# Performance work log

Hardware: AMD Instinct MI355X
Metric: run time of the kernel (lower is better)

Reference implementation:

```python
import jax, jax.numpy as jnp
import numpy as np

B, S, D = 1, 2048, 1024
H, HD = 16, 64            # attn_num, head dim (D = H*HD)
TE, K, ED = 16, 2, 512    # experts, top_k, expert_dim
DS = 2048                 # shared_expert_dim
EPS = 1e-5
THETA = 10000.0
RSF = 1.0                 # routed_scaling_factor


def rmsnorm(x, w):
    return x * jax.lax.rsqrt(jnp.mean(x * x, axis=-1, keepdims=True) + EPS) * w


def rope(x):
    # x: [B,H,S,a]; half-split rotary as in RotaryEmb
    a = x.shape[-1]
    inv = (1.0 / THETA) ** (jnp.arange(0, a, 2, dtype=jnp.float32) / a)
    fr = jnp.outer(jnp.arange(x.shape[2], dtype=jnp.float32), inv)[None, None]  # [1,1,S,a/2]
    c, s = jnp.cos(fr), jnp.sin(fr)
    x1, x2 = jnp.split(x, 2, axis=-1)
    return jnp.concatenate([x1 * c + x2 * s, -x1 * s + x2 * c], axis=-1)


def setup_inputs() -> dict:
    key = jax.random.key(0)
    ks = jax.random.split(key, 16)
    w = 0.02
    return {
        "x_input": jax.random.normal(ks[0], (B, S, D), jnp.float32),
        "indices": jax.random.randint(ks[1], (B * S, K), 0, TE),
        "values": jax.random.normal(ks[2], (B * S, K), jnp.float32),
        "attn_w": jax.random.normal(ks[3], (3 * D, D), jnp.float32) * w,
        "attn_o_w": jax.random.normal(ks[4], (D, D), jnp.float32) * w,
        "attn_norm_w": jnp.ones((D,), jnp.float32),
        "ffn_norm_w": jnp.ones((D,), jnp.float32),
        "ffn_experts": jax.random.normal(ks[5], (3, TE, D, ED), jnp.float32) * w,
        "main_keys": jax.random.normal(ks[6], (D, TE), jnp.float32) * w,
        "main_bias": jnp.zeros((TE,), jnp.float32),
        "output_coeff": jnp.ones((1, 1, D), jnp.float32),
        "ffn_up_w": jax.random.normal(ks[7], (2 * DS, D), jnp.float32) * w,
        "ffn_down_w": jax.random.normal(ks[8], (D, DS), jnp.float32) * w,
        "shared_norm_w": jnp.ones((D,), jnp.float32),
    }


def reference(x_input, indices, values, attn_w, attn_o_w, attn_norm_w, ffn_norm_w,
              ffn_experts, main_keys, main_bias, output_coeff, ffn_up_w,
              ffn_down_w, shared_norm_w):
    # --- attention block ---
    x = rmsnorm(x_input, attn_norm_w)
    qkv = x @ attn_w.T                                  # [B,S,3D]
    xq, xk, xv = jnp.split(qkv, 3, axis=-1)
    def heads(t):
        return t.reshape(B, S, H, HD).transpose(0, 2, 1, 3)  # [B,H,S,HD]
    q, k, v = rope(heads(xq)), rope(heads(xk)), heads(xv)
    att = jnp.einsum('bhqa,bhka->bhqk', q, k) / jnp.sqrt(jnp.float32(HD))
    causal = jnp.tril(jnp.ones((S, S), bool))
    att = jnp.where(causal, att, jnp.finfo(att.dtype).min)
    att = jax.nn.softmax(att, axis=-1)
    o = jnp.einsum('bhqk,bhka->bhqa', att, v)
    x_attn = o.transpose(0, 2, 1, 3).reshape(B, S, D)
    x_ffn_input = x_attn @ attn_o_w.T + x_input

    # --- router ---
    x_ffn = rmsnorm(x_ffn_input, ffn_norm_w)
    T = B * S
    token_values = (x_ffn @ main_keys).reshape(T, TE)
    tv = jnp.take_along_axis(token_values, indices, axis=-1)  # [T,K]
    vals = values + tv + main_bias[indices]
    scores = jax.nn.softmax(vals, axis=-1) * RSF              # [T,K]

    # --- grouped GEMM experts (SwiGLU), dense combine over experts ---
    combine = jnp.zeros((T, TE), x_ffn.dtype).at[
        jnp.arange(T)[:, None], indices].add(scores)          # [T,TE]
    xf = x_ffn.reshape(T, D)
    h1 = jnp.einsum('td,edh->eth', xf, ffn_experts[0])
    h2 = jnp.einsum('td,edh->eth', xf, ffn_experts[1])
    g = jax.nn.silu(h1) * h2                                  # [TE,T,ED]
    ye = jnp.einsum('eth,edh->etd', g, ffn_experts[2])        # [TE,T,D]
    y = jnp.einsum('etd,te->td', ye, combine).reshape(B, S, D)
    y = y * output_coeff

    # --- shared SwiGLU expert ---
    x1, x2 = jnp.split(x_ffn @ ffn_up_w.T, 2, axis=-1)
    y_shared = (jax.nn.silu(x1) * x2) @ ffn_down_w.T
    y_shared = rmsnorm(y_shared, shared_norm_w)

    return y + y_shared + x_ffn_input
```

## Files before the change

kernel.cpp:

```cpp
#include <hip/hip_runtime.h>
#include <hip/hip_bf16.h>

using bf16 = __hip_bfloat16;

#define S_   2048
#define D_   1024
#define H_   16
#define HD_  64
#define TE_  16
#define ED_  512
#define DS_  2048
#define CAP_ 512

#define NEG_ -1e30f

typedef __attribute__((ext_vector_type(8))) short bf16x8;
typedef __attribute__((ext_vector_type(4))) float f32x4;
#define MFMA16(a, b, c) __builtin_amdgcn_mfma_f32_16x16x32_bf16(a, b, c, 0, 0, 0)

__device__ __forceinline__ void storeF(float* p, float v) { *p = v; }
__device__ __forceinline__ void storeF(bf16* p, float v)  { *p = __float2bfloat16(v); }
__device__ __forceinline__ short cvt1(float f) {
    bf16 h = __float2bfloat16(f);
    return *(short*)&h;
}
__device__ __forceinline__ float b2f(short s) {
    return __uint_as_float(((unsigned)(unsigned short)s) << 16);
}

__device__ __forceinline__ void load16(const bf16* g, short* l) {
    __builtin_amdgcn_global_load_lds(
        (const __attribute__((address_space(1))) unsigned*)g,
        (__attribute__((address_space(3))) unsigned*)l, 16, 0, 0);
}

__global__ __launch_bounds__(256) void convert_kernel(
        const float* __restrict__ src, bf16* __restrict__ dst)
{
    const size_t i = ((size_t)blockIdx.x*256 + threadIdx.x)*8;
    const float4 f0 = *(const float4*)(src + i);
    const float4 f1 = *(const float4*)(src + i + 4);
    short t8[8];
    t8[0]=cvt1(f0.x); t8[1]=cvt1(f0.y); t8[2]=cvt1(f0.z); t8[3]=cvt1(f0.w);
    t8[4]=cvt1(f1.x); t8[5]=cvt1(f1.y); t8[6]=cvt1(f1.z); t8[7]=cvt1(f1.w);
    *(bf16x8*)(dst + i) = *(bf16x8*)t8;
}

__global__ __launch_bounds__(256) void mkT_kernel(
        const float* __restrict__ mk, float* __restrict__ mkT)
{
    const int idx = blockIdx.x*256 + threadIdx.x;
    const int e = idx >> 10, d = idx & 1023;
    mkT[idx] = mk[d*TE_ + e];
}

__global__ __launch_bounds__(256) void rmsnorm_kernel(
        const float* __restrict__ x, const float* __restrict__ w,
        bf16* __restrict__ out)
{
    const int t = blockIdx.x, tid = threadIdx.x;
    __shared__ float red[4];
    float xv[4];
    float ss = 0.f;
#pragma unroll
    for (int i = 0; i < 4; ++i) {
        xv[i] = x[(size_t)t*D_ + tid + 256*i];
        ss += xv[i]*xv[i];
    }
#pragma unroll
    for (int off = 32; off; off >>= 1) ss += __shfl_xor(ss, off, 64);
    if ((tid & 63) == 0) red[tid >> 6] = ss;
    __syncthreads();
    const float rn = rsqrtf((red[0]+red[1]+red[2]+red[3]) * (1.f/D_) + 1e-5f);
#pragma unroll
    for (int i = 0; i < 4; ++i) {
        const int d = tid + 256*i;
        out[(size_t)t*D_ + d] = __float2bfloat16(xv[i] * rn * w[d]);
    }
}

template<typename OutT, bool HAS_RES>
__global__ __launch_bounds__(256) void gemm_mfma_bb_kernel(
    const bf16* __restrict__ A, const bf16* __restrict__ B,
    OutT* __restrict__ C, const float* __restrict__ Res,
    int M, int N, int K)
{
    __shared__ short As[128*32];
    __shared__ short Bs[128*32];
    const int tid = threadIdx.x;
    const int w = tid >> 6, l = tid & 63;
    const int wm = w >> 1, wn = w & 1;
    const int m0 = blockIdx.y * 128, n0 = blockIdx.x * 128;
    const int lr = l >> 2, lq = l & 3;
    const int fm = l & 15, fq = l >> 4;
    f32x4 acc[4][4];
#pragma unroll
    for (int i = 0; i < 4; ++i)
#pragma unroll
        for (int j = 0; j < 4; ++j) acc[i][j] = (f32x4){0.f,0.f,0.f,0.f};

    const bf16* ga = A + (size_t)(m0 + w*16 + lr)*K + lq*8;
    const bf16* gb = B + (size_t)(n0 + w*16 + lr)*K + lq*8;
    for (int k0 = 0; k0 < K; k0 += 32) {
        load16(ga + k0,                &As[(w*16)*32]);
        load16(ga + k0 + (size_t)64*K, &As[(64 + w*16)*32]);
        load16(gb + k0,                &Bs[(w*16)*32]);
        load16(gb + k0 + (size_t)64*K, &Bs[(64 + w*16)*32]);
        __syncthreads();
        bf16x8 af[4], bfr[4];
#pragma unroll
        for (int mi = 0; mi < 4; ++mi)
            af[mi] = *(const bf16x8*)&As[(wm*64 + mi*16 + fm)*32 + fq*8];
#pragma unroll
        for (int ni = 0; ni < 4; ++ni)
            bfr[ni] = *(const bf16x8*)&Bs[(wn*64 + ni*16 + fm)*32 + fq*8];
#pragma unroll
        for (int mi = 0; mi < 4; ++mi)
#pragma unroll
            for (int ni = 0; ni < 4; ++ni)
                acc[mi][ni] = MFMA16(af[mi], bfr[ni], acc[mi][ni]);
        __syncthreads();
    }
#pragma unroll
    for (int mi = 0; mi < 4; ++mi)
#pragma unroll
        for (int ni = 0; ni < 4; ++ni)
#pragma unroll
            for (int r = 0; r < 4; ++r) {
                const int row = m0 + wm*64 + mi*16 + fq*4 + r;
                const int col = n0 + wn*64 + ni*16 + fm;
                float v = acc[mi][ni][r];
                if constexpr (HAS_RES) v += Res[(size_t)row*N + col];
                storeF(&C[(size_t)row*N + col], v);
            }
}

__global__ __launch_bounds__(256) void transpose_kernel(
    const float* __restrict__ src, bf16* __restrict__ dst)
{
    __shared__ bf16 tile[64][65];
    const int h0 = blockIdx.x*64, d0 = blockIdx.y*64, m = blockIdx.z;
    const float* s = src + (size_t)m*D_*ED_;
    bf16*        o = dst + (size_t)m*ED_*D_;
    const int tid = threadIdx.x;
#pragma unroll
    for (int i = 0; i < 16; ++i) {
        const int idx = tid + 256*i;
        const int r = idx >> 6, c = idx & 63;
        tile[r][c] = __float2bfloat16(s[(size_t)(d0 + r)*ED_ + h0 + c]);
    }
    __syncthreads();
#pragma unroll
    for (int i = 0; i < 16; ++i) {
        const int idx = tid + 256*i;
        const int r = idx >> 6, c = idx & 63;
        o[(size_t)(h0 + r)*D_ + d0 + c] = tile[c][r];
    }
}

__global__ __launch_bounds__(256) void expert_mid_mfma_kernel(
    const bf16* __restrict__ xffn, const bf16* __restrict__ w0t,
    const int* __restrict__ counts, const int* __restrict__ pairs,
    const float* __restrict__ pw, bf16* __restrict__ gbuf)
{
    const int ht = blockIdx.x, pt = blockIdx.y, e = blockIdx.z;
    const int cnt = counts[e];
    if (pt*128 >= cnt) return;
    __shared__ short Xs[128*32];
    __shared__ short W0s[64*32];
    __shared__ short W1s[64*32];
    __shared__ int   toks[128];
    __shared__ float wrow[128];
    const int tid = threadIdx.x;
    const int w = tid >> 6, l = tid & 63;
    const int wm = w >> 1, wn = w & 1;
    const int lr = l >> 2, lq = l & 3;
    const int fm = l & 15, fq = l >> 4;
    if (tid < 128) {
        const int p = pt*128 + tid;
        if (p < cnt) { toks[tid] = pairs[e*CAP_ + p] >> 1; wrow[tid] = pw[e*CAP_ + p]; }
        else         { toks[tid] = 0;                      wrow[tid] = 0.f; }
    }
    __syncthreads();
    const int t0 = toks[w*16 + lr], t1 = toks[64 + w*16 + lr];
    const bf16* gx0 = xffn + (size_t)t0*D_ + lq*8;
    const bf16* gx1 = xffn + (size_t)t1*D_ + lq*8;
    const bf16* g0  = w0t + ((size_t)e*ED_ + ht*64 + w*16 + lr)*D_ + lq*8;
    const bf16* g1  = w0t + ((size_t)(16 + e)*ED_ + ht*64 + w*16 + lr)*D_ + lq*8;
    f32x4 acc1[4][2], acc2[4][2];
#pragma unroll
    for (int i = 0; i < 4; ++i)
#pragma unroll
        for (int j = 0; j < 2; ++j) {
            acc1[i][j] = (f32x4){0.f,0.f,0.f,0.f};
            acc2[i][j] = (f32x4){0.f,0.f,0.f,0.f};
        }
    for (int k0 = 0; k0 < D_; k0 += 32) {
        load16(gx0 + k0, &Xs[(w*16)*32]);
        load16(gx1 + k0, &Xs[(64 + w*16)*32]);
        load16(g0 + k0,  &W0s[(w*16)*32]);
        load16(g1 + k0,  &W1s[(w*16)*32]);
        __syncthreads();
        bf16x8 af[4], b0[2], b1[2];
#pragma unroll
        for (int mi = 0; mi < 4; ++mi)
            af[mi] = *(const bf16x8*)&Xs[(wm*64 + mi*16 + fm)*32 + fq*8];
#pragma unroll
        for (int ni = 0; ni < 2; ++ni) {
            b0[ni] = *(const bf16x8*)&W0s[(wn*32 + ni*16 + fm)*32 + fq*8];
            b1[ni] = *(const bf16x8*)&W1s[(wn*32 + ni*16 + fm)*32 + fq*8];
        }
#pragma unroll
        for (int mi = 0; mi < 4; ++mi)
#pragma unroll
            for (int ni = 0; ni < 2; ++ni) {
                acc1[mi][ni] = MFMA16(af[mi], b0[ni], acc1[mi][ni]);
                acc2[mi][ni] = MFMA16(af[mi], b1[ni], acc2[mi][ni]);
            }
        __syncthreads();
    }
#pragma unroll
    for (int mi = 0; mi < 4; ++mi)
#pragma unroll
        for (int ni = 0; ni < 2; ++ni)
#pragma unroll
            for (int r = 0; r < 4; ++r) {
                const int row = wm*64 + mi*16 + fq*4 + r;
                const int col = wn*32 + ni*16 + fm;
                const float h1 = acc1[mi][ni][r], h2 = acc2[mi][ni][r];
                const float g = wrow[row] * (h1 / (1.f + __expf(-h1))) * h2;
                gbuf[((size_t)e*CAP_ + pt*128 + row)*ED_ + ht*64 + col] = __float2bfloat16(g);
            }
}

__global__ __launch_bounds__(256) void expert_down_mfma_kernel(
    const bf16* __restrict__ gbuf, const bf16* __restrict__ w2,
    const int* __restrict__ counts, const int* __restrict__ pairs,
    bf16* __restrict__ ytk)
{
    const int nt = blockIdx.x, pt = blockIdx.y, e = blockIdx.z;
    const int cnt = counts[e];
    if (pt*128 >= cnt) return;
    __shared__ short As[128*32];
    __shared__ short Bs[128*32];
    __shared__ int prs[128];
    const int tid = threadIdx.x;
    const int w = tid >> 6, l = tid & 63;
    const int wm = w >> 1, wn = w & 1;
    const int lr = l >> 2, lq = l & 3;
    const int fm = l & 15, fq = l >> 4;
    if (tid < 128) {
        const int p = pt*128 + tid;
        prs[tid] = (p < cnt) ? pairs[e*CAP_ + p] : -1;
    }
    __syncthreads();
    const bf16* ga = gbuf + ((size_t)e*CAP_ + pt*128 + w*16 + lr)*ED_ + lq*8;
    const bf16* gb = w2 + (size_t)e*D_*ED_ + (size_t)(nt*128 + w*16 + lr)*ED_ + lq*8;
    f32x4 acc[4][4];
#pragma unroll
    for (int i = 0; i < 4; ++i)
#pragma unroll
        for (int j = 0; j < 4; ++j) acc[i][j] = (f32x4){0.f,0.f,0.f,0.f};
    for (int k0 = 0; k0 < ED_; k0 += 32) {
        load16(ga + k0,                  &As[(w*16)*32]);
        load16(ga + k0 + (size_t)64*ED_, &As[(64 + w*16)*32]);
        load16(gb + k0,                  &Bs[(w*16)*32]);
        load16(gb + k0 + (size_t)64*ED_, &Bs[(64 + w*16)*32]);
        __syncthreads();
        bf16x8 af[4], bfr[4];
#pragma unroll
        for (int mi = 0; mi < 4; ++mi)
            af[mi] = *(const bf16x8*)&As[(wm*64 + mi*16 + fm)*32 + fq*8];
#pragma unroll
        for (int ni = 0; ni < 4; ++ni)
            bfr[ni] = *(const bf16x8*)&Bs[(wn*64 + ni*16 + fm)*32 + fq*8];
#pragma unroll
        for (int mi = 0; mi < 4; ++mi)
#pragma unroll
            for (int ni = 0; ni < 4; ++ni)
                acc[mi][ni] = MFMA16(af[mi], bfr[ni], acc[mi][ni]);
        __syncthreads();
    }
#pragma unroll
    for (int mi = 0; mi < 4; ++mi)
#pragma unroll
        for (int r = 0; r < 4; ++r) {
            const int pr = prs[wm*64 + mi*16 + fq*4 + r];
            if (pr < 0) continue;
#pragma unroll
            for (int ni = 0; ni < 4; ++ni) {
                const int col = nt*128 + wn*64 + ni*16 + fm;
                ytk[(size_t)pr*D_ + col] = __float2bfloat16(acc[mi][ni][r]);
            }
        }
}

__global__ __launch_bounds__(256) void rope_kernel(const bf16* __restrict__ qkv,
        bf16* __restrict__ qr, bf16* __restrict__ kswz)
{
    const int s = blockIdx.x, tid = threadIdx.x;
    const int c = s & 63, jt = s >> 6;
    for (int it = tid; it < 512; it += 256) {
        const int h = it >> 5, i = it & 31;
        const float inv = exp2f(-(float)i * 0.41524101186091903f);
        const float fr = (float)s * inv;
        float sn, cs;
        sincosf(fr, &sn, &cs);
        const size_t qb = (size_t)s*3072 + h*64 + i;
        const float q1 = __bfloat162float(qkv[qb]);
        const float q2 = __bfloat162float(qkv[qb + 32]);
        const size_t ob = ((size_t)h*S_ + s)*64 + i;
        qr[ob]      = __float2bfloat16(0.125f*( q1*cs + q2*sn));
        qr[ob + 32] = __float2bfloat16(0.125f*(-q1*sn + q2*cs));
        const float k1 = __bfloat162float(qkv[qb + 1024]);
        const float k2 = __bfloat162float(qkv[qb + 1024 + 32]);
        const size_t kb = ((size_t)(h*32 + jt))*4096 + (size_t)c*64;
        const int j0 = (i >> 3) ^ (c & 7);
        const int j1 = (4 + (i >> 3)) ^ (c & 7);
        kswz[kb + j0*8 + (i & 7)] = __float2bfloat16( k1*cs + k2*sn);
        kswz[kb + j1*8 + (i & 7)] = __float2bfloat16(-k1*sn + k2*cs);
    }
}

__global__ __launch_bounds__(256) void vtrans_kernel(
    const bf16* __restrict__ qkv, bf16* __restrict__ vswz)
{
    const int jt = blockIdx.x, h = blockIdx.y;
    __shared__ short Vt[64][72];
    const int tid = threadIdx.x;
#pragma unroll
    for (int it = 0; it < 2; ++it) {
        const int idx = it*256 + tid;
        const int cc = idx >> 3, seg = idx & 7;
        *(bf16x8*)&Vt[cc][seg*8] =
            *(const bf16x8*)(qkv + (size_t)(jt*64 + cc)*3072 + 2048 + h*64 + seg*8);
    }
    __syncthreads();
    bf16* out = vswz + ((size_t)(h*32 + jt))*4096;
#pragma unroll
    for (int it = 0; it < 2; ++it) {
        const int q = it*256 + tid;
        const int a = q >> 3, jo = q & 7;
        const int j = jo ^ (a & 7);
        short t8[8];
#pragma unroll
        for (int e = 0; e < 8; ++e) t8[e] = Vt[j*8 + e][a];
        *(bf16x8*)(out + a*64 + jo*8) = *(bf16x8*)t8;
    }
}

__global__ __launch_bounds__(512) void attn_mfma_kernel(
    const bf16* __restrict__ qr, const bf16* __restrict__ kswz,
    const bf16* __restrict__ vswz, bf16* __restrict__ xattn)
{
    const int p = blockIdx.x, h = blockIdx.y;
    __shared__ short Ks[2][2][4096];
    __shared__ short Vs[2][2][4096];
    __shared__ short Ps[2][64][72];
    __shared__ float Oc[64][64];
    __shared__ float Mc[64], Lc[64];
    const int tid = threadIdx.x;
    const int w = tid >> 6, l = tid & 63;
    const int g = w >> 2, gw = w & 3;
    const int fm = l & 15, fq = l >> 4;
    const int sr = gw * 16;
    const bf16* ktile = kswz + (size_t)h*32*4096;
    const bf16* vtile = vswz + (size_t)h*32*4096;

    auto stageKV = [&](int jtile, int bufidx) {
        const bf16* ks_ = ktile + (size_t)jtile*4096 + gw*1024 + l*8;
        const bf16* vs_ = vtile + (size_t)jtile*4096 + gw*1024 + l*8;
        short* kd_ = &Ks[g][bufidx][gw*1024];
        short* vd_ = &Vs[g][bufidx][gw*1024];
        load16(ks_,       kd_);
        load16(ks_ + 512, kd_ + 512);
        load16(vs_,       vd_);
        load16(vs_ + 512, vd_ + 512);
    };

    for (int half = 0; half < 2; ++half) {
        const int qt = half ? (31 - p) : p;
        const bf16* gq = qr + ((size_t)h*S_ + qt*64 + sr + fm)*64 + fq*8;
        const bf16x8 aq0 = *(const bf16x8*)gq;
        const bf16x8 aq1 = *(const bf16x8*)(gq + 32);
        f32x4 Oa[4];
        float m_i[4], l_i[4];
#pragma unroll
        for (int i = 0; i < 4; ++i) {
            Oa[i] = (f32x4){0.f,0.f,0.f,0.f};
            m_i[i] = NEG_; l_i[i] = 0.f;
        }
        const int nj = qt + 1;
        const int itmax = (nj + 1) >> 1;
        if (g < nj) stageKV(g, 0);
        __syncthreads();
        for (int it = 0; it < itmax; ++it) {
            const int jt = g + 2*it;
            const int buf = it & 1;
            if (jt + 2 < nj) stageKV(jt + 2, buf ^ 1);
            if (jt < nj) {
                const short* kb = &Ks[g][buf][0];
                const short* vb = &Vs[g][buf][0];
                f32x4 sc[4];
#pragma unroll
                for (int ni = 0; ni < 4; ++ni) sc[ni] = (f32x4){0.f,0.f,0.f,0.f};
                __builtin_amdgcn_s_setprio(1);
#pragma unroll
                for (int ni = 0; ni < 4; ++ni) {
                    const int row = ni*16 + fm;
                    bf16x8 bk0 = *(const bf16x8*)&kb[row*64 + (( fq      ^ (fm & 7))<<3)];
                    bf16x8 bk1 = *(const bf16x8*)&kb[row*64 + (((fq + 4) ^ (fm & 7))<<3)];
                    sc[ni] = MFMA16(aq0, bk0, sc[ni]);
                    sc[ni] = MFMA16(aq1, bk1, sc[ni]);
                }
                __builtin_amdgcn_s_setprio(0);
                const bool diag = (jt == qt);
#pragma unroll
                for (int r = 0; r < 4; ++r) {
                    const int rowin = sr + fq*4 + r;
                    float rm = NEG_;
#pragma unroll
                    for (int ni = 0; ni < 4; ++ni) {
                        if (diag && (ni*16 + fm) > rowin) sc[ni][r] = NEG_;
                        rm = fmaxf(rm, sc[ni][r]);
                    }
                    rm = fmaxf(rm, __shfl_xor(rm, 1, 16));
                    rm = fmaxf(rm, __shfl_xor(rm, 2, 16));
                    rm = fmaxf(rm, __shfl_xor(rm, 4, 16));
                    rm = fmaxf(rm, __shfl_xor(rm, 8, 16));
                    const float mnew  = fmaxf(m_i[r], rm);
                    const float alpha = __expf(m_i[r] - mnew);
                    float rs = 0.f;
#pragma unroll
                    for (int ni = 0; ni < 4; ++ni) {
                        const float pv = __expf(sc[ni][r] - mnew);
                        sc[ni][r] = pv; rs += pv;
                    }
                    rs += __shfl_xor(rs, 1, 16);
                    rs += __shfl_xor(rs, 2, 16);
                    rs += __shfl_xor(rs, 4, 16);
                    rs += __shfl_xor(rs, 8, 16);
                    l_i[r] = l_i[r]*alpha + rs;
                    m_i[r] = mnew;
#pragma unroll
                    for (int ni = 0; ni < 4; ++ni) Oa[ni][r] *= alpha;
                }
#pragma unroll
                for (int ni = 0; ni < 4; ++ni)
#pragma unroll
                    for (int r = 0; r < 4; ++r)
                        Ps[g][sr + fq*4 + r][ni*16 + fm] = cvt1(sc[ni][r]);
                bf16x8 ap0 = *(const bf16x8*)&Ps[g][sr + fm][fq*8];
                bf16x8 ap1 = *(const bf16x8*)&Ps[g][sr + fm][32 + fq*8];
                __builtin_amdgcn_s_setprio(1);
#pragma unroll
                for (int ni = 0; ni < 4; ++ni) {
                    const int row = ni*16 + fm;
                    bf16x8 bv0 = *(const bf16x8*)&vb[row*64 + (( fq      ^ (fm & 7))<<3)];
                    bf16x8 bv1 = *(const bf16x8*)&vb[row*64 + (((fq + 4) ^ (fm & 7))<<3)];
                    Oa[ni] = MFMA16(ap0, bv0, Oa[ni]);
                    Oa[ni] = MFMA16(ap1, bv1, Oa[ni]);
                }
                __builtin_amdgcn_s_setprio(0);
            }
            __syncthreads();
        }
        if (g == 1) {
#pragma unroll
            for (int r = 0; r < 4; ++r) {
                const int row = sr + fq*4 + r;
                if (fm == 0) { Mc[row] = m_i[r]; Lc[row] = l_i[r]; }
#pragma unroll
                for (int ni = 0; ni < 4; ++ni) Oc[row][ni*16 + fm] = Oa[ni][r];
            }
        }
        __syncthreads();
        if (g == 0) {
#pragma unroll
            for (int r = 0; r < 4; ++r) {
                const int row = sr + fq*4 + r;
                const float m1 = Mc[row], l1 = Lc[row];
                const float mm = fmaxf(m_i[r], m1);
                const float a0 = __expf(m_i[r] - mm), a1 = __expf(m1 - mm);
                const float inv = 1.f / (l_i[r]*a0 + l1*a1);
                const int srow = qt*64 + row;
#pragma unroll
                for (int ni = 0; ni < 4; ++ni)
                    xattn[(size_t)srow*D_ + h*64 + ni*16 + fm] =
                        __float2bfloat16((Oa[ni][r]*a0 + Oc[row][ni*16 + fm]*a1)*inv);
            }
        }
        __syncthreads();
    }
}

__global__ __launch_bounds__(256) void router_kernel(
    const bf16* __restrict__ xffn, const int* __restrict__ indices,
    const float* __restrict__ values, const float* __restrict__ mkT,
    const float* __restrict__ mbias, int* __restrict__ counts,
    int* __restrict__ pairs, float* __restrict__ pw)
{
    const int wv = threadIdx.x >> 6, lane = threadIdx.x & 63;
    const int t = blockIdx.x*4 + wv;
    const int i0 = indices[t*2], i1 = indices[t*2 + 1];
    const bf16* xp = xffn + (size_t)t*D_ + lane*16;
    const bf16x8 xa = *(const bf16x8*)xp;
    const bf16x8 xb = *(const bf16x8*)(xp + 8);
    float xv[16];
#pragma unroll
    for (int j = 0; j < 8; ++j) { xv[j] = b2f(xa[j]); xv[8 + j] = b2f(xb[j]); }
    const float* k0 = mkT + (size_t)i0*D_ + lane*16;
    const float* k1 = mkT + (size_t)i1*D_ + lane*16;
    float a0[16], a1[16];
#pragma unroll
    for (int j = 0; j < 4; ++j) {
        *(float4*)&a0[j*4] = *(const float4*)(k0 + j*4);
        *(float4*)&a1[j*4] = *(const float4*)(k1 + j*4);
    }
    float s0 = 0.f, s1 = 0.f;
#pragma unroll
    for (int j = 0; j < 16; ++j) {
        s0 = fmaf(xv[j], a0[j], s0);
        s1 = fmaf(xv[j], a1[j], s1);
    }
#pragma unroll
    for (int off = 32; off; off >>= 1) {
        s0 += __shfl_xor(s0, off, 64);
        s1 += __shfl_xor(s1, off, 64);
    }
    if (lane == 0) {
        const float v0 = values[t*2]     + s0 + mbias[i0];
        const float v1 = values[t*2 + 1] + s1 + mbias[i1];
        const float mx = fmaxf(v0, v1);
        const float e0 = __expf(v0 - mx), e1 = __expf(v1 - mx);
        const float inv = 1.f / (e0 + e1);
        const int p0 = atomicAdd(&counts[i0], 1);
        if (p0 < CAP_) { pairs[i0*CAP_ + p0] = t*2;     pw[i0*CAP_ + p0] = e0*inv; }
        const int p1 = atomicAdd(&counts[i1], 1);
        if (p1 < CAP_) { pairs[i1*CAP_ + p1] = t*2 + 1; pw[i1*CAP_ + p1] = e1*inv; }
    }
}

__global__ __launch_bounds__(256) void silu_mul_kernel(const bf16* __restrict__ u,
        bf16* __restrict__ gsh)
{
    const int idx = blockIdx.x*256 + threadIdx.x;
    const int t = idx >> 11, j = idx & 2047;
    const float a = __bfloat162float(u[(size_t)t*(2*DS_) + j]);
    const float b = __bfloat162float(u[(size_t)t*(2*DS_) + DS_ + j]);
    gsh[idx] = __float2bfloat16(a / (1.f + __expf(-a)) * b);
}

__global__ __launch_bounds__(256) void final_kernel(
    const bf16* __restrict__ ytk, const float* __restrict__ ysh,
    const float* __restrict__ xffin, const float* __restrict__ coeff,
    const float* __restrict__ shw, float* __restrict__ out)
{
    const int t = blockIdx.x, tid = threadIdx.x;
    __shared__ float red[4];
    float yv[4];
    float ss = 0.f;
#pragma unroll
    for (int i = 0; i < 4; ++i) {
        yv[i] = ysh[(size_t)t*D_ + tid + 256*i];
        ss += yv[i]*yv[i];
    }
#pragma unroll
    for (int off = 32; off; off >>= 1) ss += __shfl_xor(ss, off, 64);
    if ((tid & 63) == 0) red[tid >> 6] = ss;
    __syncthreads();
    const float rn = rsqrtf((red[0]+red[1]+red[2]+red[3]) * (1.f/D_) + 1e-5f);
#pragma unroll
    for (int i = 0; i < 4; ++i) {
        const int d = tid + 256*i;
        const float y = (__bfloat162float(ytk[(size_t)(t*2)*D_ + d])
                       + __bfloat162float(ytk[(size_t)(t*2 + 1)*D_ + d])) * coeff[d];
        out[(size_t)t*D_ + d] = y + yv[i]*rn*shw[d] + xffin[(size_t)t*D_ + d];
    }
}

extern "C" void kernel_launch(void* const* d_in, const int* in_sizes, int n_in,
                              void* d_out, int out_size, void* d_ws, size_t ws_size,
                              hipStream_t stream)
{
    const float* x_input     = (const float*)d_in[0];
    const int*   indices     = (const int*)  d_in[1];
    const float* values      = (const float*)d_in[2];
    const float* attn_w      = (const float*)d_in[3];
    const float* attn_o_w    = (const float*)d_in[4];
    const float* attn_norm_w = (const float*)d_in[5];
    const float* ffn_norm_w  = (const float*)d_in[6];
    const float* ffn_experts = (const float*)d_in[7];
    const float* main_keys   = (const float*)d_in[8];
    const float* main_bias   = (const float*)d_in[9];
    const float* out_coeff   = (const float*)d_in[10];
    const float* ffn_up_w    = (const float*)d_in[11];
    const float* ffn_down_w  = (const float*)d_in[12];
    const float* shared_nw   = (const float*)d_in[13];

    char* wp = (char*)d_ws;
    auto alloc = [&](size_t n) { char* p = wp; wp += (n + 255) & ~(size_t)255; return p; };
    char*  regA   = alloc(28*1024*1024 + 4096);
    bf16*  xn     = (bf16*)(regA);
    bf16*  qkv    = (bf16*)(regA + 4*1024*1024);
    bf16*  qr     = (bf16*)(regA + 16*1024*1024);
    bf16*  xattn  = (bf16*)(regA + 20*1024*1024);
    bf16*  w2bf   = (bf16*)(regA);
    bf16*  u      = (bf16*)(regA);
    bf16*  gsh    = (bf16*)(regA + 16*1024*1024);
    float* xffin  = (float*)alloc((size_t)S_*D_*4);
    bf16*  kswz   = (bf16*)xffin;
    bf16*  vswz   = kswz + (size_t)H_*32*4096;
    bf16*  xffn   = (bf16*) alloc((size_t)S_*D_*2);
    int*   counts = (int*)  alloc(TE_*4);
    int*   pairs  = (int*)  alloc((size_t)TE_*CAP_*4);
    float* pwgt   = (float*)alloc((size_t)TE_*CAP_*4);
    float* mkT    = (float*)alloc((size_t)TE_*D_*4);
    bf16*  gbuf   = (bf16*) alloc((size_t)TE_*CAP_*ED_*2);
    bf16*  o_bf   = (bf16*)gbuf;
    float* ysh    = (float*)((char*)gbuf);
    bf16*  ytk    = (bf16*) alloc((size_t)S_*2*D_*2);
    bf16*  awbf   = (bf16*)ytk;
    bf16*  w0t    = (bf16*) alloc((size_t)2*TE_*ED_*D_*2);
    bf16*  upbf   = (bf16*)w0t;
    bf16*  dnbf   = (bf16*)((char*)w0t + 8*1024*1024);

    hipMemsetAsync(counts, 0, TE_*4, stream);

    transpose_kernel<<<dim3(ED_/64, D_/64, 2*TE_), 256, 0, stream>>>(ffn_experts, w0t);
    convert_kernel<<<(3*D_*D_)/2048, 256, 0, stream>>>(attn_w, awbf);
    convert_kernel<<<(D_*D_)/2048, 256, 0, stream>>>(attn_o_w, o_bf);
    mkT_kernel<<<(TE_*D_)/256, 256, 0, stream>>>(main_keys, mkT);

    rmsnorm_kernel<<<S_, 256, 0, stream>>>(x_input, attn_norm_w, xn);
    gemm_mfma_bb_kernel<bf16,false><<<dim3(3*D_/128, S_/128), 256, 0, stream>>>(
        xn, awbf, qkv, nullptr, S_, 3*D_, D_);
    rope_kernel<<<S_, 256, 0, stream>>>(qkv, qr, kswz);
    vtrans_kernel<<<dim3(S_/64, H_), 256, 0, stream>>>(qkv, vswz);
    convert_kernel<<<(TE_*D_*ED_)/2048, 256, 0, stream>>>(
        ffn_experts + (size_t)2*TE_*D_*ED_, w2bf);
    attn_mfma_kernel<<<dim3(16, H_), 512, 0, stream>>>(qr, kswz, vswz, xattn);
    gemm_mfma_bb_kernel<float,true><<<dim3(D_/128, S_/128), 256, 0, stream>>>(
        xattn, o_bf, xffin, x_input, S_, D_, D_);

    rmsnorm_kernel<<<S_, 256, 0, stream>>>(xffin, ffn_norm_w, xffn);
    router_kernel<<<S_/4, 256, 0, stream>>>(xffn, indices, values, mkT, main_bias,
                                            counts, pairs, pwgt);
    expert_mid_mfma_kernel<<<dim3(ED_/64, CAP_/128, TE_), 256, 0, stream>>>(
        xffn, w0t, counts, pairs, pwgt, gbuf);
    convert_kernel<<<(2*DS_*D_)/2048, 256, 0, stream>>>(ffn_up_w, upbf);
    convert_kernel<<<(D_*DS_)/2048, 256, 0, stream>>>(ffn_down_w, dnbf);
    expert_down_mfma_kernel<<<dim3(D_/128, CAP_/128, TE_), 256, 0, stream>>>(
        gbuf, w2bf, counts, pairs, ytk);

    gemm_mfma_bb_kernel<bf16,false><<<dim3(2*DS_/128, S_/128), 256, 0, stream>>>(
        xffn, upbf, u, nullptr, S_, 2*DS_, D_);
    silu_mul_kernel<<<(S_*DS_)/256, 256, 0, stream>>>(u, gsh);
    gemm_mfma_bb_kernel<float,false><<<dim3(D_/128, S_/128), 256, 0, stream>>>(
        gsh, dnbf, ysh, nullptr, S_, D_, DS_);

    final_kernel<<<S_, 256, 0, stream>>>(ytk, ysh, xffin, out_coeff, shared_nw,
                                         (float*)d_out);
}
```

Before: 516.6 us.

## Double-buffer LDS tiles in GEMM/expert kernels and vectorize elementwise kernels

The dense GEMM and both expert GEMM kernels now use two LDS buffers: they prefetch the next K-slice with global_load_lds while issuing MFMAs on the current slice, which removes one barrier per iteration and hides load latency. The rmsnorm, silu_mul and final kernels switch to float4 and bf16x8/bf16x4 vector loads and stores. silu_mul now launches eight times fewer blocks to match the wider per-thread work. Doubling the LDS footprint per block may lower occupancy.

After: 509.5 us. About the same (-1.4%).

```diff
diff --git a/kernel.cpp b/kernel.cpp
--- a/kernel.cpp
+++ b/kernel.cpp
@@ -15,6 +15,7 @@
 #define NEG_ -1e30f
 
 typedef __attribute__((ext_vector_type(8))) short bf16x8;
+typedef __attribute__((ext_vector_type(4))) short bf16x4;
 typedef __attribute__((ext_vector_type(4))) float f32x4;
 #define MFMA16(a, b, c) __builtin_amdgcn_mfma_f32_16x16x32_bf16(a, b, c, 0, 0, 0)
 
@@ -60,23 +61,18 @@
 {
     const int t = blockIdx.x, tid = threadIdx.x;
     __shared__ float red[4];
-    float xv[4];
-    float ss = 0.f;
-#pragma unroll
-    for (int i = 0; i < 4; ++i) {
-        xv[i] = x[(size_t)t*D_ + tid + 256*i];
-        ss += xv[i]*xv[i];
-    }
+    const float4 xv = *(const float4*)(x + (size_t)t*D_ + tid*4);
+    float ss = xv.x*xv.x + xv.y*xv.y + xv.z*xv.z + xv.w*xv.w;
 #pragma unroll
     for (int off = 32; off; off >>= 1) ss += __shfl_xor(ss, off, 64);
     if ((tid & 63) == 0) red[tid >> 6] = ss;
     __syncthreads();
     const float rn = rsqrtf((red[0]+red[1]+red[2]+red[3]) * (1.f/D_) + 1e-5f);
-#pragma unroll
-    for (int i = 0; i < 4; ++i) {
-        const int d = tid + 256*i;
-        out[(size_t)t*D_ + d] = __float2bfloat16(xv[i] * rn * w[d]);
-    }
+    const float4 wv = *(const float4*)(w + tid*4);
+    short o[4];
+    o[0] = cvt1(xv.x*rn*wv.x); o[1] = cvt1(xv.y*rn*wv.y);
+    o[2] = cvt1(xv.z*rn*wv.z); o[3] = cvt1(xv.w*rn*wv.w);
+    *(bf16x4*)(out + (size_t)t*D_ + tid*4) = *(bf16x4*)o;
 }
 
 template<typename OutT, bool HAS_RES>
@@ -85,8 +81,8 @@
     OutT* __restrict__ C, const float* __restrict__ Res,
     int M, int N, int K)
 {
-    __shared__ short As[128*32];
-    __shared__ short Bs[128*32];
+    __shared__ short As[2][128*32];
+    __shared__ short Bs[2][128*32];
     const int tid = threadIdx.x;
     const int w = tid >> 6, l = tid & 63;
     const int wm = w >> 1, wn = w & 1;
@@ -101,19 +97,28 @@
 
     const bf16* ga = A + (size_t)(m0 + w*16 + lr)*K + lq*8;
     const bf16* gb = B + (size_t)(n0 + w*16 + lr)*K + lq*8;
-    for (int k0 = 0; k0 < K; k0 += 32) {
-        load16(ga + k0,                &As[(w*16)*32]);
-        load16(ga + k0 + (size_t)64*K, &As[(64 + w*16)*32]);
-        load16(gb + k0,                &Bs[(w*16)*32]);
-        load16(gb + k0 + (size_t)64*K, &Bs[(64 + w*16)*32]);
-        __syncthreads();
+    load16(ga,                &As[0][(w*16)*32]);
+    load16(ga + (size_t)64*K, &As[0][(64 + w*16)*32]);
+    load16(gb,                &Bs[0][(w*16)*32]);
+    load16(gb + (size_t)64*K, &Bs[0][(64 + w*16)*32]);
+    __syncthreads();
+    const int nk = K >> 5;
+    for (int t = 0; t < nk; ++t) {
+        const int cur = t & 1;
+        if (t + 1 < nk) {
+            const int k1 = (t + 1) << 5;
+            load16(ga + k1,                &As[cur^1][(w*16)*32]);
+            load16(ga + k1 + (size_t)64*K, &As[cur^1][(64 + w*16)*32]);
+            load16(gb + k1,                &Bs[cur^1][(w*16)*32]);
+            load16(gb + k1 + (size_t)64*K, &Bs[cur^1][(64 + w*16)*32]);
+        }
         bf16x8 af[4], bfr[4];
 #pragma unroll
         for (int mi = 0; mi < 4; ++mi)
-            af[mi] = *(const bf16x8*)&As[(wm*64 + mi*16 + fm)*32 + fq*8];
+            af[mi] = *(const bf16x8*)&As[cur][(wm*64 + mi*16 + fm)*32 + fq*8];
 #pragma unroll
         for (int ni = 0; ni < 4; ++ni)
-            bfr[ni] = *(const bf16x8*)&Bs[(wn*64 + ni*16 + fm)*32 + fq*8];
+            bfr[ni] = *(const bf16x8*)&Bs[cur][(wn*64 + ni*16 + fm)*32 + fq*8];
 #pragma unroll
         for (int mi = 0; mi < 4; ++mi)
 #pragma unroll
@@ -166,9 +171,9 @@
     const int ht = blockIdx.x, pt = blockIdx.y, e = blockIdx.z;
     const int cnt = counts[e];
     if (pt*128 >= cnt) return;
-    __shared__ short Xs[128*32];
-    __shared__ short W0s[64*32];
-    __shared__ short W1s[64*32];
+    __shared__ short Xs[2][128*32];
+    __shared__ short W0s[2][64*32];
+    __shared__ short W1s[2][64*32];
     __shared__ int   toks[128];
     __shared__ float wrow[128];
     const int tid = threadIdx.x;
@@ -195,20 +200,29 @@
             acc1[i][j] = (f32x4){0.f,0.f,0.f,0.f};
             acc2[i][j] = (f32x4){0.f,0.f,0.f,0.f};
         }
-    for (int k0 = 0; k0 < D_; k0 += 32) {
-        load16(gx0 + k0, &Xs[(w*16)*32]);
-        load16(gx1 + k0, &Xs[(64 + w*16)*32]);
-        load16(g0 + k0,  &W0s[(w*16)*32]);
-        load16(g1 + k0,  &W1s[(w*16)*32]);
-        __syncthreads();
+    load16(gx0, &Xs[0][(w*16)*32]);
+    load16(gx1, &Xs[0][(64 + w*16)*32]);
+    load16(g0,  &W0s[0][(w*16)*32]);
+    load16(g1,  &W1s[0][(w*16)*32]);
+    __syncthreads();
+    const int nk = D_ >> 5;
+    for (int t = 0; t < nk; ++t) {
+        const int cur = t & 1;
+        if (t + 1 < nk) {
+            const int k1 = (t + 1) << 5;
+            load16(gx0 + k1, &Xs[cur^1][(w*16)*32]);
+            load16(gx1 + k1, &Xs[cur^1][(64 + w*16)*32]);
+            load16(g0 + k1,  &W0s[cur^1][(w*16)*32]);
+            load16(g1 + k1,  &W1s[cur^1][(w*16)*32]);
+        }
         bf16x8 af[4], b0[2], b1[2];
 #pragma unroll
         for (int mi = 0; mi < 4; ++mi)
-            af[mi] = *(const bf16x8*)&Xs[(wm*64 + mi*16 + fm)*32 + fq*8];
+            af[mi] = *(const bf16x8*)&Xs[cur][(wm*64 + mi*16 + fm)*32 + fq*8];
 #pragma unroll
         for (int ni = 0; ni < 2; ++ni) {
-            b0[ni] = *(const bf16x8*)&W0s[(wn*32 + ni*16 + fm)*32 + fq*8];
-            b1[ni] = *(const bf16x8*)&W1s[(wn*32 + ni*16 + fm)*32 + fq*8];
+            b0[ni] = *(const bf16x8*)&W0s[cur][(wn*32 + ni*16 + fm)*32 + fq*8];
+            b1[ni] = *(const bf16x8*)&W1s[cur][(wn*32 + ni*16 + fm)*32 + fq*8];
         }
 #pragma unroll
         for (int mi = 0; mi < 4; ++mi)
@@ -241,8 +255,8 @@
     const int nt = blockIdx.x, pt = blockIdx.y, e = blockIdx.z;
     const int cnt = counts[e];
     if (pt*128 >= cnt) return;
-    __shared__ short As[128*32];
-    __shared__ short Bs[128*32];
+    __shared__ short As[2][128*32];
+    __shared__ short Bs[2][128*32];
     __shared__ int prs[128];
     const int tid = threadIdx.x;
     const int w = tid >> 6, l = tid & 63;
@@ -261,19 +275,28 @@
     for (int i = 0; i < 4; ++i)
 #pragma unroll
         for (int j = 0; j < 4; ++j) acc[i][j] = (f32x4){0.f,0.f,0.f,0.f};
-    for (int k0 = 0; k0 < ED_; k0 += 32) {
-        load16(ga + k0,                  &As[(w*16)*32]);
-        load16(ga + k0 + (size_t)64*ED_, &As[(64 + w*16)*32]);
-        load16(gb + k0,                  &Bs[(w*16)*32]);
-        load16(gb + k0 + (size_t)64*ED_, &Bs[(64 + w*16)*32]);
-        __syncthreads();
+    load16(ga,                  &As[0][(w*16)*32]);
+    load16(ga + (size_t)64*ED_, &As[0][(64 + w*16)*32]);
+    load16(gb,                  &Bs[0][(w*16)*32]);
+    load16(gb + (size_t)64*ED_, &Bs[0][(64 + w*16)*32]);
+    __syncthreads();
+    const int nk = ED_ >> 5;
+    for (int t = 0; t < nk; ++t) {
+        const int cur = t & 1;
+        if (t + 1 < nk) {
+            const int k1 = (t + 1) << 5;
+            load16(ga + k1,                  &As[cur^1][(w*16)*32]);
+            load16(ga + k1 + (size_t)64*ED_, &As[cur^1][(64 + w*16)*32]);
+            load16(gb + k1,                  &Bs[cur^1][(w*16)*32]);
+            load16(gb + k1 + (size_t)64*ED_, &Bs[cur^1][(64 + w*16)*32]);
+        }
         bf16x8 af[4], bfr[4];
 #pragma unroll
         for (int mi = 0; mi < 4; ++mi)
-            af[mi] = *(const bf16x8*)&As[(wm*64 + mi*16 + fm)*32 + fq*8];
+            af[mi] = *(const bf16x8*)&As[cur][(wm*64 + mi*16 + fm)*32 + fq*8];
 #pragma unroll
         for (int ni = 0; ni < 4; ++ni)
-            bfr[ni] = *(const bf16x8*)&Bs[(wn*64 + ni*16 + fm)*32 + fq*8];
+            bfr[ni] = *(const bf16x8*)&Bs[cur][(wn*64 + ni*16 + fm)*32 + fq*8];
 #pragma unroll
         for (int mi = 0; mi < 4; ++mi)
 #pragma unroll
@@ -545,10 +568,16 @@
         bf16* __restrict__ gsh)
 {
     const int idx = blockIdx.x*256 + threadIdx.x;
-    const int t = idx >> 11, j = idx & 2047;
-    const float a = __bfloat162float(u[(size_t)t*(2*DS_) + j]);
-    const float b = __bfloat162float(u[(size_t)t*(2*DS_) + DS_ + j]);
-    gsh[idx] = __float2bfloat16(a / (1.f + __expf(-a)) * b);
+    const int t = idx >> 8, j = idx & 255;
+    const bf16x8 av = *(const bf16x8*)(u + (size_t)t*(2*DS_) + j*8);
+    const bf16x8 bv = *(const bf16x8*)(u + (size_t)t*(2*DS_) + DS_ + j*8);
+    short o[8];
+#pragma unroll
+    for (int k = 0; k < 8; ++k) {
+        const float a = b2f(av[k]), b = b2f(bv[k]);
+        o[k] = cvt1(a / (1.f + __expf(-a)) * b);
+    }
+    *(bf16x8*)(gsh + (size_t)idx*8) = *(bf16x8*)o;
 }
 
 __global__ __launch_bounds__(256) void final_kernel(
@@ -558,25 +587,25 @@
 {
     const int t = blockIdx.x, tid = threadIdx.x;
     __shared__ float red[4];
-    float yv[4];
-    float ss = 0.f;
-#pragma unroll
-    for (int i = 0; i < 4; ++i) {
-        yv[i] = ysh[(size_t)t*D_ + tid + 256*i];
-        ss += yv[i]*yv[i];
-    }
+    const float4 yv = *(const float4*)(ysh + (size_t)t*D_ + tid*4);
+    float ss = yv.x*yv.x + yv.y*yv.y + yv.z*yv.z + yv.w*yv.w;
 #pragma unroll
     for (int off = 32; off; off >>= 1) ss += __shfl_xor(ss, off, 64);
     if ((tid & 63) == 0) red[tid >> 6] = ss;
     __syncthreads();
     const float rn = rsqrtf((red[0]+red[1]+red[2]+red[3]) * (1.f/D_) + 1e-5f);
-#pragma unroll
-    for (int i = 0; i < 4; ++i) {
-        const int d = tid + 256*i;
-        const float y = (__bfloat162float(ytk[(size_t)(t*2)*D_ + d])
-                       + __bfloat162float(ytk[(size_t)(t*2 + 1)*D_ + d])) * coeff[d];
-        out[(size_t)t*D_ + d] = y + yv[i]*rn*shw[d] + xffin[(size_t)t*D_ + d];
-    }
+    const int d = tid*4;
+    const bf16x4 y0 = *(const bf16x4*)(ytk + (size_t)(t*2)*D_ + d);
+    const bf16x4 y1 = *(const bf16x4*)(ytk + (size_t)(t*2 + 1)*D_ + d);
+    const float4 cf = *(const float4*)(coeff + d);
+    const float4 sw = *(const float4*)(shw + d);
+    const float4 xf = *(const float4*)(xffin + (size_t)t*D_ + d);
+    float4 o;
+    o.x = (b2f(y0[0]) + b2f(y1[0]))*cf.x + yv.x*rn*sw.x + xf.x;
+    o.y = (b2f(y0[1]) + b2f(y1[1]))*cf.y + yv.y*rn*sw.y + xf.y;
+    o.z = (b2f(y0[2]) + b2f(y1[2]))*cf.z + yv.z*rn*sw.z + xf.z;
+    o.w = (b2f(y0[3]) + b2f(y1[3]))*cf.w + yv.w*rn*sw.w + xf.w;
+    *(float4*)(out + (size_t)t*D_ + d) = o;
 }
 
 extern "C" void kernel_launch(void* const* d_in, const int* in_sizes, int n_in,
@@ -655,7 +684,7 @@
 
     gemm_mfma_bb_kernel<bf16,false><<<dim3(2*DS_/128, S_/128), 256, 0, stream>>>(
         xffn, upbf, u, nullptr, S_, 2*DS_, D_);
-    silu_mul_kernel<<<(S_*DS_)/256, 256, 0, stream>>>(u, gsh);
+    silu_mul_kernel<<<(S_*DS_)/2048, 256, 0, stream>>>(u, gsh);
     gemm_mfma_bb_kernel<float,false><<<dim3(D_/128, S_/128), 256, 0, stream>>>(
         gsh, dnbf, ysh, nullptr, S_, D_, DS_);
 
```
